# Kernel tuning notes

Measured on AMD Instinct MI355X. Metric: run time of the kernel, lower is better.

## Reference

```python
import jax, jax.numpy as jnp
import numpy as np

H = 2          # h_dim (hard-coded in PPIModel)
L = 4          # n_hid rgcn layers
R = 16         # num_rels
B = 8          # num_bases
N = 1_000_000  # num_nodes
E = 16_000_000 # num_edges


def setup_inputs() -> dict:
    key = jax.random.key(0)
    ks = jax.random.split(key, 10)
    features = jax.random.normal(ks[0], (N * H,), dtype=jnp.float32)
    edge_src = jax.random.randint(ks[1], (E,), 0, N)
    edge_dst = jax.random.randint(ks[2], (E,), 0, N)
    edge_type = jax.random.randint(ks[3], (E,), 0, R)
    norm = jax.random.uniform(ks[4], (E, 1), dtype=jnp.float32)
    # Basis-decomposition params per layer: W_r = sum_b comp[r,b] * V[b]
    V = jax.random.normal(ks[5], (L, B, H, H), dtype=jnp.float32) / np.sqrt(H)
    comp = jax.random.normal(ks[6], (L, R, B), dtype=jnp.float32) / np.sqrt(B)
    bias = jnp.zeros((L, H), dtype=jnp.float32)  # DGL RelGraphConv h_bias (default bias=True)
    w_mlp = jax.random.normal(ks[7], (1, N * H), dtype=jnp.float32) / np.sqrt(N * H)
    b_mlp = jnp.zeros((1,), dtype=jnp.float32)
    return dict(features=features, norm=norm, V=V, comp=comp, bias=bias,
                w_mlp=w_mlp, b_mlp=b_mlp,
                edge_src=edge_src, edge_dst=edge_dst, edge_type=edge_type)


def reference(features, norm, V, comp, bias, w_mlp, b_mlp, edge_src, edge_dst, edge_type):
    x = features.reshape(-1, H)          # [N, 2]
    skip = x
    for i in range(L):
        # relation weights from bases: [R, H, H]
        W = jnp.einsum('rb,bio->rio', comp[i], V[i])
        # message per edge: gather src feats, apply relation weight, scale by norm
        msg = jnp.einsum('ei,eio->eo', x[edge_src], W[edge_type]) * norm  # [E, 2]
        # scatter-sum to destination nodes
        h = jax.ops.segment_sum(msg, edge_dst, num_segments=N) + bias[i]  # [N, 2]
        if i < L - 1:
            h = jax.nn.relu(h)
        x = h
        if i % 2 == 1:
            x = x + skip
            skip = x
    flat = x.reshape(1, N * H)           # [1, 2N]
    logit = flat @ w_mlp.T + b_mlp       # [1, 1]
    return jax.nn.sigmoid(logit)
```

## Files before the change

### kernel.cpp

```cpp
#include <hip/hip_runtime.h>
#include <hip/hip_bf16.h>
#include <hip/hip_fp16.h>

#define HD 2
#define LAYERS 4
#define RELS 16
#define BASES 8

#define NB   512
#define BSH  11
#define SBLK 512
#define TPB  256


__global__ void prep_kernel(const float* __restrict__ V, const float* __restrict__ comp,
                            float* __restrict__ W, float* __restrict__ acc) {
    int idx = threadIdx.x;
    if (idx < LAYERS * RELS * 4) {
        int l  = idx >> 6;
        int r  = (idx >> 2) & (RELS - 1);
        int io = idx & 3;
        float s = 0.f;
        for (int b = 0; b < BASES; ++b)
            s += comp[(l * RELS + r) * BASES + b] * V[(l * BASES + b) * 4 + io];
        W[idx] = s;
    }
    if (idx == 0) *acc = 0.f;
}

__global__ void finalize_kernel(const float* __restrict__ acc,
                                const float* __restrict__ b_mlp,
                                float* __restrict__ out) {
    float v = *acc + b_mlp[0];
    out[0] = 1.f / (1.f + expf(-v));
}

__global__ __launch_bounds__(TPB) void f2h_kernel(const float2* __restrict__ f,
                                                  __half2* __restrict__ h, int N) {
    int i = blockIdx.x * TPB + threadIdx.x;
    int stride = gridDim.x * TPB;
    for (; i < N; i += stride)
        h[i] = __float22half2_rn(f[i]);
}


__global__ __launch_bounds__(TPB) void hist_kernel(const int* __restrict__ dst,
                                                   unsigned* __restrict__ blockhist,
                                                   int E, int per) {
    __shared__ unsigned hist[NB];
    for (int i = threadIdx.x; i < NB; i += TPB) hist[i] = 0u;
    __syncthreads();
    int blk = blockIdx.x;
    int e0 = blk * per;
    int e1 = min(e0 + per, E);
    const int4* dst4 = (const int4*)dst;
    int g0 = e0 >> 2, g1 = e1 >> 2;
    for (int g = g0 + threadIdx.x; g < g1; g += TPB) {
        int4 d = dst4[g];
        atomicAdd(&hist[((unsigned)d.x) >> BSH], 1u);
        atomicAdd(&hist[((unsigned)d.y) >> BSH], 1u);
        atomicAdd(&hist[((unsigned)d.z) >> BSH], 1u);
        atomicAdd(&hist[((unsigned)d.w) >> BSH], 1u);
    }
    for (int e = (g1 << 2) + threadIdx.x; e < e1; e += TPB)
        atomicAdd(&hist[((unsigned)dst[e]) >> BSH], 1u);
    __syncthreads();
    for (int i = threadIdx.x; i < NB; i += TPB)
        blockhist[(size_t)blk * NB + i] = hist[i];
}

__global__ __launch_bounds__(TPB) void colscan_kernel(unsigned* __restrict__ blockhist,
                                                      unsigned* __restrict__ totals) {
    int bucket = blockIdx.x;
    int t = threadIdx.x;
    unsigned v0 = blockhist[(size_t)(2 * t)     * NB + bucket];
    unsigned v1 = blockhist[(size_t)(2 * t + 1) * NB + bucket];
    unsigned run = v0 + v1;
    __shared__ unsigned s[TPB];
    s[t] = run;
    __syncthreads();
    for (int off = 1; off < TPB; off <<= 1) {
        unsigned x = (t >= off) ? s[t - off] : 0u;
        __syncthreads();
        s[t] += x;
        __syncthreads();
    }
    unsigned base = s[t] - run;
    blockhist[(size_t)(2 * t)     * NB + bucket] = base;
    blockhist[(size_t)(2 * t + 1) * NB + bucket] = base + v0;
    if (t == TPB - 1) totals[bucket] = s[TPB - 1];
}

__global__ __launch_bounds__(TPB) void scan_kernel(const unsigned* __restrict__ totals,
                                                   unsigned* __restrict__ base) {
    int t = threadIdx.x;
    unsigned v0 = totals[2 * t];
    unsigned v1 = totals[2 * t + 1];
    unsigned run = v0 + v1;
    __shared__ unsigned s[TPB];
    s[t] = run;
    __syncthreads();
    for (int off = 1; off < TPB; off <<= 1) {
        unsigned x = (t >= off) ? s[t - off] : 0u;
        __syncthreads();
        s[t] += x;
        __syncthreads();
    }
    unsigned b0 = s[t] - run;
    base[2 * t]     = b0;
    base[2 * t + 1] = b0 + v0;
    if (t == TPB - 1) base[NB] = s[TPB - 1];
}

__global__ __launch_bounds__(TPB) void scatter_kernel(const int* __restrict__ src,
                                                      const int* __restrict__ dst,
                                                      const int* __restrict__ typ,
                                                      const float* __restrict__ norm,
                                                      const unsigned* __restrict__ blockhist,
                                                      const unsigned* __restrict__ base,
                                                      uint2* __restrict__ packed,
                                                      int E, int per) {
    __shared__ unsigned cnt[NB];
    int blk = blockIdx.x;
    for (int i = threadIdx.x; i < NB; i += TPB)
        cnt[i] = blockhist[(size_t)blk * NB + i] + base[i];
    __syncthreads();
    int e0 = blk * per;
    int e1 = min(e0 + per, E);
    const int4*   src4 = (const int4*)src;
    const int4*   dst4 = (const int4*)dst;
    const int4*   typ4 = (const int4*)typ;
    const float4* nrm4 = (const float4*)norm;
    int g0 = e0 >> 2, g1 = e1 >> 2;

#define PUT(SS, DD, TT, NN)                                                       \
    {                                                                             \
        unsigned _d = (unsigned)(DD);                                             \
        unsigned _bucket = _d >> BSH;                                             \
        unsigned _pos = atomicAdd(&cnt[_bucket], 1u);                             \
        unsigned _w1 = (_d & ((1u << BSH) - 1u)) | (((unsigned)(TT)) << 12) |     \
                       ((unsigned)__half_as_ushort(__float2half_rn(NN)) << 16);   \
        packed[_pos] = make_uint2((unsigned)(SS), _w1);                           \
    }

    for (int g = g0 + threadIdx.x; g < g1; g += TPB) {
        int4 s = src4[g];
        int4 d = dst4[g];
        int4 t = typ4[g];
        float4 nm = nrm4[g];
        PUT(s.x, d.x, t.x, nm.x)
        PUT(s.y, d.y, t.y, nm.y)
        PUT(s.z, d.z, t.z, nm.z)
        PUT(s.w, d.w, t.w, nm.w)
    }
    for (int e = (g1 << 2) + threadIdx.x; e < e1; e += TPB)
        PUT(src[e], dst[e], typ[e], norm[e])
#undef PUT
}

__global__ __launch_bounds__(TPB) void bucket_edge_kernel(
    const uint2* __restrict__ packed,
    const unsigned* __restrict__ base,
    const __half2* __restrict__ xh,
    const float* __restrict__ Wl,
    const float* __restrict__ bias2,
    const __half2* __restrict__ skiph,
    __half2* __restrict__ outh,
    const float2* __restrict__ w2,
    float* __restrict__ acc,
    int N, int do_relu)
{
    __shared__ float acc0[1 << BSH];
    __shared__ float acc1[1 << BSH];
    __shared__ float sW[64];
    __shared__ float wred[4];

    int t = threadIdx.x;
#pragma unroll
    for (int k = 0; k < (1 << BSH) / TPB; ++k) {
        acc0[k * TPB + t] = 0.f;
        acc1[k * TPB + t] = 0.f;
    }
    if (t < 64) sW[t] = Wl[t];
    __syncthreads();

    int b  = blockIdx.x;
    int e0 = (int)base[b];
    int e1 = (int)base[b + 1];

    const unsigned long long* pk8 = (const unsigned long long*)packed;

    for (int e = e0 + t; e < e1; e += 2 * TPB) {
        unsigned long long q0 = __builtin_nontemporal_load(&pk8[e]);
        int e2 = e + TPB;
        bool has2 = e2 < e1;
        unsigned long long q1 = has2 ? __builtin_nontemporal_load(&pk8[e2]) : 0ull;

        unsigned s0i = (unsigned)(q0 & 0xffffffffu);
        unsigned w10 = (unsigned)(q0 >> 32);
        unsigned s1i = (unsigned)(q1 & 0xffffffffu);
        unsigned w11 = (unsigned)(q1 >> 32);

        __half2 hv0 = xh[s0i];
        __half2 hv1 = has2 ? xh[s1i] : __half2{};

        {
            float xv0 = __low2float(hv0), xv1 = __high2float(hv0);
            unsigned dof = w10 & ((1u << BSH) - 1u);
            int wb = (int)((w10 >> 12) & 15u) << 2;
            float nm = __half2float(__ushort_as_half((unsigned short)(w10 >> 16)));
            float m0 = (xv0 * sW[wb + 0] + xv1 * sW[wb + 2]) * nm;
            float m1 = (xv0 * sW[wb + 1] + xv1 * sW[wb + 3]) * nm;
            atomicAdd(&acc0[dof], m0);
            atomicAdd(&acc1[dof], m1);
        }
        if (has2) {
            float xv0 = __low2float(hv1), xv1 = __high2float(hv1);
            unsigned dof = w11 & ((1u << BSH) - 1u);
            int wb = (int)((w11 >> 12) & 15u) << 2;
            float nm = __half2float(__ushort_as_half((unsigned short)(w11 >> 16)));
            float m0 = (xv0 * sW[wb + 0] + xv1 * sW[wb + 2]) * nm;
            float m1 = (xv0 * sW[wb + 1] + xv1 * sW[wb + 3]) * nm;
            atomicAdd(&acc0[dof], m0);
            atomicAdd(&acc1[dof], m1);
        }
    }
    __syncthreads();

    float b0 = bias2[0], b1 = bias2[1];
    int nodeBase = b << BSH;
    float part = 0.f;
#pragma unroll
    for (int k = 0; k < (1 << BSH) / TPB; ++k) {
        int i = k * TPB + t;
        int node = nodeBase + i;
        if (node < N) {
            float v0 = acc0[i] + b0;
            float v1 = acc1[i] + b1;
            if (do_relu) { v0 = fmaxf(v0, 0.f); v1 = fmaxf(v1, 0.f); }
            if (skiph) {
                __half2 sv = skiph[node];
                v0 += __low2float(sv); v1 += __high2float(sv);
            }
            if (outh) outh[node] = __float22half2_rn(make_float2(v0, v1));
            if (w2)   { float2 wv = w2[node]; part += v0 * wv.x + v1 * wv.y; }
        }
    }
    if (w2) {
        for (int off = 32; off > 0; off >>= 1) part += __shfl_down(part, off, 64);
        int lane = t & 63, wv = t >> 6;
        if (lane == 0) wred[wv] = part;
        __syncthreads();
        if (t == 0) atomicAdd(acc, wred[0] + wred[1] + wred[2] + wred[3]);
    }
}


__global__ void zero_kernel(float4* __restrict__ p, int n4) {
    int i = blockIdx.x * blockDim.x + threadIdx.x;
    int stride = gridDim.x * blockDim.x;
    for (; i < n4; i += stride) p[i] = make_float4(0.f, 0.f, 0.f, 0.f);
}

__global__ __launch_bounds__(256) void edge_kernel(
    const float* __restrict__ x, const int* __restrict__ src,
    const int* __restrict__ dst, const int* __restrict__ typ,
    const float* __restrict__ norm, const float* __restrict__ Wl,
    float* __restrict__ h, int E)
{
    __shared__ float sW[64];
    if (threadIdx.x < 64) sW[threadIdx.x] = Wl[threadIdx.x];
    __syncthreads();
    const float2* __restrict__ x2 = (const float2*)x;
    int tid = blockIdx.x * blockDim.x + threadIdx.x;
    int stride = gridDim.x * blockDim.x;
    for (int e = tid; e < E; e += stride) {
        int s = src[e], d = dst[e], t = typ[e];
        float nm = norm[e];
        float2 xv = x2[s];
        int wb = t << 2;
        float m0 = (xv.x * sW[wb + 0] + xv.y * sW[wb + 2]) * nm;
        float m1 = (xv.x * sW[wb + 1] + xv.y * sW[wb + 3]) * nm;
        atomicAdd(&h[2 * (size_t)d],     m0);
        atomicAdd(&h[2 * (size_t)d + 1], m1);
    }
}

__global__ void node_kernel(const float* __restrict__ h, const float* __restrict__ bias_l,
                            const float* __restrict__ skip, float* __restrict__ xout,
                            int N, int do_relu)
{
    float b0 = bias_l[0], b1 = bias_l[1];
    const float2* __restrict__ h2 = (const float2*)h;
    const float2* __restrict__ s2 = (const float2*)skip;
    float2* __restrict__ o2 = (float2*)xout;
    int i = blockIdx.x * blockDim.x + threadIdx.x;
    int stride = gridDim.x * blockDim.x;
    for (; i < N; i += stride) {
        float2 v = h2[i];
        v.x += b0; v.y += b1;
        if (do_relu) { v.x = fmaxf(v.x, 0.f); v.y = fmaxf(v.y, 0.f); }
        if (skip) { float2 sv = s2[i]; v.x += sv.x; v.y += sv.y; }
        o2[i] = v;
    }
}

__global__ __launch_bounds__(256) void dot_kernel(const float* __restrict__ a,
                                                  const float* __restrict__ b,
                                                  float* __restrict__ acc, int n)
{
    int i = blockIdx.x * blockDim.x + threadIdx.x;
    int stride = gridDim.x * blockDim.x;
    float s = 0.f;
    int n4 = n >> 2;
    const float4* __restrict__ a4 = (const float4*)a;
    const float4* __restrict__ b4 = (const float4*)b;
    for (int g = i; g < n4; g += stride) {
        float4 av = a4[g], bv = b4[g];
        s += av.x * bv.x + av.y * bv.y + av.z * bv.z + av.w * bv.w;
    }
    for (int e = (n4 << 2) + i; e < n; e += stride) s += a[e] * b[e];
    for (int off = 32; off > 0; off >>= 1) s += __shfl_down(s, off, 64);
    __shared__ float wsum[4];
    int lane = threadIdx.x & 63, wv = threadIdx.x >> 6;
    if (lane == 0) wsum[wv] = s;
    __syncthreads();
    if (threadIdx.x == 0) atomicAdd(acc, wsum[0] + wsum[1] + wsum[2] + wsum[3]);
}


static inline size_t align256(size_t x) { return (x + 255) & ~(size_t)255; }

extern "C" void kernel_launch(void* const* d_in, const int* in_sizes, int n_in,
                              void* d_out, int out_size, void* d_ws, size_t ws_size,
                              hipStream_t stream) {
    const float* features = (const float*)d_in[0];
    const float* norm     = (const float*)d_in[1];
    const float* V        = (const float*)d_in[2];
    const float* comp     = (const float*)d_in[3];
    const float* bias     = (const float*)d_in[4];
    const float* w_mlp    = (const float*)d_in[5];
    const float* b_mlp    = (const float*)d_in[6];
    const int*   esrc     = (const int*)d_in[7];
    const int*   edst     = (const int*)d_in[8];
    const int*   etyp     = (const int*)d_in[9];

    int NH = in_sizes[0];
    int N  = NH / 2;
    int E  = in_sizes[7];

    char* ws = (char*)d_ws;
    size_t oA    = 0;
    size_t oB    = align256(oA + (size_t)NH * 4);
    size_t oC    = align256(oB + (size_t)NH * 4);
    size_t oFH   = align256(oC + (size_t)NH * 4);
    size_t oAH   = align256(oFH + (size_t)N * 4);
    size_t oBH   = align256(oAH + (size_t)N * 4);
    size_t oCH   = align256(oBH + (size_t)N * 4);
    size_t oW    = align256(oCH + (size_t)N * 4);
    size_t oAcc  = align256(oW + 1024);
    size_t oBase = align256(oAcc + 4);
    size_t oTot  = align256(oBase + (size_t)(NB + 1) * 4);
    size_t oHist = align256(oTot + (size_t)NB * 4);
    size_t oPack = align256(oHist + (size_t)SBLK * NB * 4);
    size_t REQ   = oPack + (size_t)E * 8;

    float* A    = (float*)(ws + oA);
    float* B    = (float*)(ws + oB);
    float* C    = (float*)(ws + oC);
    float* W    = (float*)(ws + oW);
    float* acc  = (float*)(ws + oAcc);

    prep_kernel<<<1, 256, 0, stream>>>(V, comp, W, acc);

    if (ws_size >= REQ && N <= (1 << 20)) {
        __half2* FH = (__half2*)(ws + oFH);
        __half2* AH = (__half2*)(ws + oAH);
        __half2* BH = (__half2*)(ws + oBH);
        __half2* CH = (__half2*)(ws + oCH);
        unsigned* base      = (unsigned*)(ws + oBase);
        unsigned* totals    = (unsigned*)(ws + oTot);
        unsigned* blockhist = (unsigned*)(ws + oHist);
        uint2*    packed    = (uint2*)(ws + oPack);

        int per = (((E + SBLK - 1) / SBLK) + 3) & ~3;

        int cb = min((N + TPB - 1) / TPB, 2048);
        f2h_kernel    <<<cb,   TPB, 0, stream>>>((const float2*)features, FH, N);
        hist_kernel   <<<SBLK, TPB, 0, stream>>>(edst, blockhist, E, per);
        colscan_kernel<<<NB,   TPB, 0, stream>>>(blockhist, totals);
        scan_kernel   <<<1,    TPB, 0, stream>>>(totals, base);
        scatter_kernel<<<SBLK, TPB, 0, stream>>>(esrc, edst, etyp, norm,
                                                 blockhist, base, packed, E, per);

        int nbkt = (N + (1 << BSH) - 1) >> BSH;
        const float2* w2 = (const float2*)w_mlp;

        bucket_edge_kernel<<<nbkt, TPB, 0, stream>>>(packed, base, FH, W + 0,
            bias + 0, nullptr, AH, nullptr, acc, N, 1);
        bucket_edge_kernel<<<nbkt, TPB, 0, stream>>>(packed, base, AH, W + 64,
            bias + 2, FH, BH, nullptr, acc, N, 1);
        bucket_edge_kernel<<<nbkt, TPB, 0, stream>>>(packed, base, BH, W + 128,
            bias + 4, nullptr, CH, nullptr, acc, N, 1);
        bucket_edge_kernel<<<nbkt, TPB, 0, stream>>>(packed, base, CH, W + 192,
            bias + 6, BH, nullptr, w2, acc, N, 0);
    } else {
        int zb = (NH / 4 + 255) / 256;
        int eb = (E / 4 + 255) / 256;
        int nb = (N + 255) / 256;
        int db = (NH / 4 + 255) / 256;

        zero_kernel<<<zb, 256, 0, stream>>>((float4*)A, NH / 4);
        edge_kernel<<<eb, 256, 0, stream>>>(features, esrc, edst, etyp, norm, W + 0, A, E);
        node_kernel<<<nb, 256, 0, stream>>>(A, bias + 0, nullptr, A, N, 1);

        zero_kernel<<<zb, 256, 0, stream>>>((float4*)B, NH / 4);
        edge_kernel<<<eb, 256, 0, stream>>>(A, esrc, edst, etyp, norm, W + 64, B, E);
        node_kernel<<<nb, 256, 0, stream>>>(B, bias + 2, features, B, N, 1);

        zero_kernel<<<zb, 256, 0, stream>>>((float4*)C, NH / 4);
        edge_kernel<<<eb, 256, 0, stream>>>(B, esrc, edst, etyp, norm, W + 128, C, E);
        node_kernel<<<nb, 256, 0, stream>>>(C, bias + 4, nullptr, C, N, 1);

        zero_kernel<<<zb, 256, 0, stream>>>((float4*)A, NH / 4);
        edge_kernel<<<eb, 256, 0, stream>>>(C, esrc, edst, etyp, norm, W + 192, A, E);
        node_kernel<<<nb, 256, 0, stream>>>(A, bias + 6, B, A, N, 0);

        dot_kernel<<<db, 256, 0, stream>>>(A, w_mlp, acc, NH);
    }

    finalize_kernel<<<1, 1, 0, stream>>>(acc, b_mlp, (float*)d_out);
}
```

Measured before the change: 1.133 ms.

## Bucket edges by destination tile and source block for gather locality

Replaces the 512 destination buckets of 2048 nodes with a two-level key: 16K-node destination tiles, each subdivided by 2048-node source blocks, giving 32768 sort keys. Edges within a tile are then ordered by source block, which should make the per-edge feature gathers more cache-local. The edge kernel now runs one 1024-thread block per tile with larger LDS accumulators. The price is much larger histograms (128KB LDS per block, bigger blockhist and colscan work) and far fewer edge-kernel blocks (about 62), which may underfill the GPU.

```diff
diff --git a/kernel.cpp b/kernel.cpp
--- a/kernel.cpp
+++ b/kernel.cpp
@@ -7,10 +7,17 @@
 #define RELS 16
 #define BASES 8
 
-#define NB   512
-#define BSH  11
-#define SBLK 512
-#define TPB  256
+#define TSH    14
+#define TILEN  (1 << TSH)
+#define SBH    11
+#define SRCB_BITS 9
+#define KEYS   32768
+#define SBLK   192
+#define TPB    256
+#define ETPB   1024
+
+static const int KEYS_LDS_BYTES = KEYS * 4;
+static const int EDGE_LDS_BYTES = 2 * TILEN * 4;
 
 
 __global__ void prep_kernel(const float* __restrict__ V, const float* __restrict__ comp,
@@ -44,72 +51,76 @@
 }
 
 
-__global__ __launch_bounds__(TPB) void hist_kernel(const int* __restrict__ dst,
+__global__ __launch_bounds__(TPB) void hist_kernel(const int* __restrict__ src,
+                                                   const int* __restrict__ dst,
                                                    unsigned* __restrict__ blockhist,
                                                    int E, int per) {
-    __shared__ unsigned hist[NB];
-    for (int i = threadIdx.x; i < NB; i += TPB) hist[i] = 0u;
+    extern __shared__ unsigned hist[];
+    for (int i = threadIdx.x; i < KEYS; i += TPB) hist[i] = 0u;
     __syncthreads();
     int blk = blockIdx.x;
     int e0 = blk * per;
     int e1 = min(e0 + per, E);
+    const int4* src4 = (const int4*)src;
     const int4* dst4 = (const int4*)dst;
     int g0 = e0 >> 2, g1 = e1 >> 2;
     for (int g = g0 + threadIdx.x; g < g1; g += TPB) {
+        int4 s = src4[g];
         int4 d = dst4[g];
-        atomicAdd(&hist[((unsigned)d.x) >> BSH], 1u);
-        atomicAdd(&hist[((unsigned)d.y) >> BSH], 1u);
-        atomicAdd(&hist[((unsigned)d.z) >> BSH], 1u);
-        atomicAdd(&hist[((unsigned)d.w) >> BSH], 1u);
+        atomicAdd(&hist[((((unsigned)d.x) >> TSH) << SRCB_BITS) | (((unsigned)s.x) >> SBH)], 1u);
+        atomicAdd(&hist[((((unsigned)d.y) >> TSH) << SRCB_BITS) | (((unsigned)s.y) >> SBH)], 1u);
+        atomicAdd(&hist[((((unsigned)d.z) >> TSH) << SRCB_BITS) | (((unsigned)s.z) >> SBH)], 1u);
+        atomicAdd(&hist[((((unsigned)d.w) >> TSH) << SRCB_BITS) | (((unsigned)s.w) >> SBH)], 1u);
     }
     for (int e = (g1 << 2) + threadIdx.x; e < e1; e += TPB)
-        atomicAdd(&hist[((unsigned)dst[e]) >> BSH], 1u);
-    __syncthreads();
-    for (int i = threadIdx.x; i < NB; i += TPB)
-        blockhist[(size_t)blk * NB + i] = hist[i];
-}
-
-__global__ __launch_bounds__(TPB) void colscan_kernel(unsigned* __restrict__ blockhist,
-                                                      unsigned* __restrict__ totals) {
-    int bucket = blockIdx.x;
+        atomicAdd(&hist[((((unsigned)dst[e]) >> TSH) << SRCB_BITS) | (((unsigned)src[e]) >> SBH)], 1u);
+    __syncthreads();
+    for (int i = threadIdx.x; i < KEYS; i += TPB)
+        blockhist[(size_t)blk * KEYS + i] = hist[i];
+}
+
+__global__ __launch_bounds__(64) void colscan_kernel(unsigned* __restrict__ blockhist,
+                                                     unsigned* __restrict__ totals) {
+    int key = blockIdx.x;
     int t = threadIdx.x;
-    unsigned v0 = blockhist[(size_t)(2 * t)     * NB + bucket];
-    unsigned v1 = blockhist[(size_t)(2 * t + 1) * NB + bucket];
-    unsigned run = v0 + v1;
-    __shared__ unsigned s[TPB];
-    s[t] = run;
-    __syncthreads();
-    for (int off = 1; off < TPB; off <<= 1) {
-        unsigned x = (t >= off) ? s[t - off] : 0u;
-        __syncthreads();
-        s[t] += x;
-        __syncthreads();
-    }
-    unsigned base = s[t] - run;
-    blockhist[(size_t)(2 * t)     * NB + bucket] = base;
-    blockhist[(size_t)(2 * t + 1) * NB + bucket] = base + v0;
-    if (t == TPB - 1) totals[bucket] = s[TPB - 1];
-}
-
-__global__ __launch_bounds__(TPB) void scan_kernel(const unsigned* __restrict__ totals,
-                                                   unsigned* __restrict__ base) {
+    unsigned v0 = blockhist[(size_t)(3 * t)     * KEYS + key];
+    unsigned v1 = blockhist[(size_t)(3 * t + 1) * KEYS + key];
+    unsigned v2 = blockhist[(size_t)(3 * t + 2) * KEYS + key];
+    unsigned run = v0 + v1 + v2;
+    unsigned v = run;
+    for (int o = 1; o < 64; o <<= 1) {
+        unsigned u = __shfl_up(v, o, 64);
+        if (t >= o) v += u;
+    }
+    unsigned excl = v - run;
+    blockhist[(size_t)(3 * t)     * KEYS + key] = excl;
+    blockhist[(size_t)(3 * t + 1) * KEYS + key] = excl + v0;
+    blockhist[(size_t)(3 * t + 2) * KEYS + key] = excl + v0 + v1;
+    if (t == 63) totals[key] = v;
+}
+
+__global__ __launch_bounds__(ETPB) void scan_kernel(const unsigned* __restrict__ totals,
+                                                    unsigned* __restrict__ base) {
+    __shared__ unsigned wpart[ETPB / 64];
     int t = threadIdx.x;
-    unsigned v0 = totals[2 * t];
-    unsigned v1 = totals[2 * t + 1];
-    unsigned run = v0 + v1;
-    __shared__ unsigned s[TPB];
-    s[t] = run;
-    __syncthreads();
-    for (int off = 1; off < TPB; off <<= 1) {
-        unsigned x = (t >= off) ? s[t - off] : 0u;
-        __syncthreads();
-        s[t] += x;
-        __syncthreads();
-    }
-    unsigned b0 = s[t] - run;
-    base[2 * t]     = b0;
-    base[2 * t + 1] = b0 + v0;
-    if (t == TPB - 1) base[NB] = s[TPB - 1];
+    unsigned run = 0;
+    for (int k = 0; k < 32; ++k) run += totals[t * 32 + k];
+    unsigned lane = t & 63, wv = t >> 6;
+    unsigned v = run;
+    for (int o = 1; o < 64; o <<= 1) {
+        unsigned u = __shfl_up(v, o, 64);
+        if (lane >= (unsigned)o) v += u;
+    }
+    if (lane == 63) wpart[wv] = v;
+    __syncthreads();
+    unsigned wbase = 0;
+    for (int w = 0; w < (int)(ETPB / 64); ++w) if ((unsigned)w < wv) wbase += wpart[w];
+    unsigned e = wbase + v - run;
+    for (int k = 0; k < 32; ++k) {
+        base[t * 32 + k] = e;
+        e += totals[t * 32 + k];
+    }
+    if (t == ETPB - 1) base[KEYS] = e;
 }
 
 __global__ __launch_bounds__(TPB) void scatter_kernel(const int* __restrict__ src,
@@ -120,10 +131,10 @@
                                                       const unsigned* __restrict__ base,
                                                       uint2* __restrict__ packed,
                                                       int E, int per) {
-    __shared__ unsigned cnt[NB];
+    extern __shared__ unsigned cnt[];
     int blk = blockIdx.x;
-    for (int i = threadIdx.x; i < NB; i += TPB)
-        cnt[i] = blockhist[(size_t)blk * NB + i] + base[i];
+    for (int i = threadIdx.x; i < KEYS; i += TPB)
+        cnt[i] = blockhist[(size_t)blk * KEYS + i] + base[i];
     __syncthreads();
     int e0 = blk * per;
     int e1 = min(e0 + per, E);
@@ -133,14 +144,17 @@
     const float4* nrm4 = (const float4*)norm;
     int g0 = e0 >> 2, g1 = e1 >> 2;
 
-#define PUT(SS, DD, TT, NN)                                                       \
-    {                                                                             \
-        unsigned _d = (unsigned)(DD);                                             \
-        unsigned _bucket = _d >> BSH;                                             \
-        unsigned _pos = atomicAdd(&cnt[_bucket], 1u);                             \
-        unsigned _w1 = (_d & ((1u << BSH) - 1u)) | (((unsigned)(TT)) << 12) |     \
-                       ((unsigned)__half_as_ushort(__float2half_rn(NN)) << 16);   \
-        packed[_pos] = make_uint2((unsigned)(SS), _w1);                           \
+#define PUT(SS, DD, TT, NN)                                                        \
+    {                                                                              \
+        unsigned _s = (unsigned)(SS);                                              \
+        unsigned _d = (unsigned)(DD);                                              \
+        unsigned _key = ((_d >> TSH) << SRCB_BITS) | (_s >> SBH);                  \
+        unsigned _pos = atomicAdd(&cnt[_key], 1u);                                 \
+        unsigned _doff = _d & (TILEN - 1u);                                        \
+        unsigned _w0 = _s | (((unsigned)(TT)) << 20) | ((_doff & 0xFFu) << 24);    \
+        unsigned _w1 = (_doff >> 8) |                                              \
+                       ((unsigned)__half_as_ushort(__float2half_rn(NN)) << 16);    \
+        packed[_pos] = make_uint2(_w0, _w1);                                       \
     }
 
     for (int g = g0 + threadIdx.x; g < g1; g += TPB) {
@@ -158,8 +172,8 @@
 #undef PUT
 }
 
-__global__ __launch_bounds__(TPB) void bucket_edge_kernel(
-    const uint2* __restrict__ packed,
+__global__ __launch_bounds__(ETPB) void edge_tile_kernel(
+    const unsigned long long* __restrict__ rec8,
     const unsigned* __restrict__ base,
     const __half2* __restrict__ xh,
     const float* __restrict__ Wl,
@@ -170,69 +184,43 @@
     float* __restrict__ acc,
     int N, int do_relu)
 {
-    __shared__ float acc0[1 << BSH];
-    __shared__ float acc1[1 << BSH];
+    extern __shared__ float dsm[];
+    float* acc0 = dsm;
+    float* acc1 = dsm + TILEN;
     __shared__ float sW[64];
-    __shared__ float wred[4];
+    __shared__ float wred[ETPB / 64];
 
     int t = threadIdx.x;
-#pragma unroll
-    for (int k = 0; k < (1 << BSH) / TPB; ++k) {
-        acc0[k * TPB + t] = 0.f;
-        acc1[k * TPB + t] = 0.f;
-    }
+    for (int i = t; i < TILEN; i += ETPB) { acc0[i] = 0.f; acc1[i] = 0.f; }
     if (t < 64) sW[t] = Wl[t];
     __syncthreads();
 
-    int b  = blockIdx.x;
-    int e0 = (int)base[b];
-    int e1 = (int)base[b + 1];
-
-    const unsigned long long* pk8 = (const unsigned long long*)packed;
-
-    for (int e = e0 + t; e < e1; e += 2 * TPB) {
-        unsigned long long q0 = __builtin_nontemporal_load(&pk8[e]);
-        int e2 = e + TPB;
-        bool has2 = e2 < e1;
-        unsigned long long q1 = has2 ? __builtin_nontemporal_load(&pk8[e2]) : 0ull;
-
-        unsigned s0i = (unsigned)(q0 & 0xffffffffu);
-        unsigned w10 = (unsigned)(q0 >> 32);
-        unsigned s1i = (unsigned)(q1 & 0xffffffffu);
-        unsigned w11 = (unsigned)(q1 >> 32);
-
-        __half2 hv0 = xh[s0i];
-        __half2 hv1 = has2 ? xh[s1i] : __half2{};
-
-        {
-            float xv0 = __low2float(hv0), xv1 = __high2float(hv0);
-            unsigned dof = w10 & ((1u << BSH) - 1u);
-            int wb = (int)((w10 >> 12) & 15u) << 2;
-            float nm = __half2float(__ushort_as_half((unsigned short)(w10 >> 16)));
-            float m0 = (xv0 * sW[wb + 0] + xv1 * sW[wb + 2]) * nm;
-            float m1 = (xv0 * sW[wb + 1] + xv1 * sW[wb + 3]) * nm;
-            atomicAdd(&acc0[dof], m0);
-            atomicAdd(&acc1[dof], m1);
-        }
-        if (has2) {
-            float xv0 = __low2float(hv1), xv1 = __high2float(hv1);
-            unsigned dof = w11 & ((1u << BSH) - 1u);
-            int wb = (int)((w11 >> 12) & 15u) << 2;
-            float nm = __half2float(__ushort_as_half((unsigned short)(w11 >> 16)));
-            float m0 = (xv0 * sW[wb + 0] + xv1 * sW[wb + 2]) * nm;
-            float m1 = (xv0 * sW[wb + 1] + xv1 * sW[wb + 3]) * nm;
-            atomicAdd(&acc0[dof], m0);
-            atomicAdd(&acc1[dof], m1);
-        }
+    int tile = blockIdx.x;
+    unsigned e0 = base[tile << SRCB_BITS];
+    unsigned e1 = base[min((tile + 1) << SRCB_BITS, KEYS)];
+
+    for (unsigned e = e0 + t; e < e1; e += ETPB) {
+        unsigned long long q = __builtin_nontemporal_load(&rec8[e]);
+        unsigned w0 = (unsigned)q;
+        unsigned w1 = (unsigned)(q >> 32);
+        unsigned src  = w0 & 0xFFFFFu;
+        int      wb   = (int)((w0 >> 20) & 15u) << 2;
+        unsigned doff = (w0 >> 24) | ((w1 & 0x3Fu) << 8);
+        float    nm   = __half2float(__ushort_as_half((unsigned short)(w1 >> 16)));
+        __half2  hv   = xh[src];
+        float x0 = __low2float(hv), x1 = __high2float(hv);
+        float m0 = (x0 * sW[wb + 0] + x1 * sW[wb + 2]) * nm;
+        float m1 = (x0 * sW[wb + 1] + x1 * sW[wb + 3]) * nm;
+        atomicAdd(&acc0[doff], m0);
+        atomicAdd(&acc1[doff], m1);
     }
     __syncthreads();
 
     float b0 = bias2[0], b1 = bias2[1];
-    int nodeBase = b << BSH;
+    int nodeBase = tile << TSH;
     float part = 0.f;
-#pragma unroll
-    for (int k = 0; k < (1 << BSH) / TPB; ++k) {
-        int i = k * TPB + t;
+    for (int k = 0; k < TILEN / ETPB; ++k) {
+        int i = k * ETPB + t;
         int node = nodeBase + i;
         if (node < N) {
             float v0 = acc0[i] + b0;
@@ -247,11 +235,14 @@
         }
     }
     if (w2) {
-        for (int off = 32; off > 0; off >>= 1) part += __shfl_down(part, off, 64);
-        int lane = t & 63, wv = t >> 6;
-        if (lane == 0) wred[wv] = part;
+        for (int o = 32; o > 0; o >>= 1) part += __shfl_down(part, o, 64);
+        if ((t & 63) == 0) wred[t >> 6] = part;
         __syncthreads();
-        if (t == 0) atomicAdd(acc, wred[0] + wred[1] + wred[2] + wred[3]);
+        if (t == 0) {
+            float s = 0.f;
+            for (int w = 0; w < (int)(ETPB / 64); ++w) s += wred[w];
+            atomicAdd(acc, s);
+        }
     }
 }
 
@@ -350,26 +341,24 @@
     int E  = in_sizes[7];
 
     char* ws = (char*)d_ws;
-    size_t oA    = 0;
-    size_t oB    = align256(oA + (size_t)NH * 4);
-    size_t oC    = align256(oB + (size_t)NH * 4);
-    size_t oFH   = align256(oC + (size_t)NH * 4);
+    size_t oW    = 0;
+    size_t oAcc  = align256(oW + 1024);
+    size_t oBase = align256(oAcc + 4);
+    size_t oTot  = align256(oBase + (size_t)(KEYS + 1) * 4);
+    size_t oFH   = align256(oTot + (size_t)KEYS * 4);
     size_t oAH   = align256(oFH + (size_t)N * 4);
     size_t oBH   = align256(oAH + (size_t)N * 4);
     size_t oCH   = align256(oBH + (size_t)N * 4);
-    size_t oW    = align256(oCH + (size_t)N * 4);
-    size_t oAcc  = align256(oW + 1024);
-    size_t oBase = align256(oAcc + 4);
-    size_t oTot  = align256(oBase + (size_t)(NB + 1) * 4);
-    size_t oHist = align256(oTot + (size_t)NB * 4);
-    size_t oPack = align256(oHist + (size_t)SBLK * NB * 4);
+    size_t oHist = align256(oCH + (size_t)N * 4);
+    size_t oPack = align256(oHist + (size_t)SBLK * KEYS * 4);
     size_t REQ   = oPack + (size_t)E * 8;
 
-    float* A    = (float*)(ws + oA);
-    float* B    = (float*)(ws + oB);
-    float* C    = (float*)(ws + oC);
-    float* W    = (float*)(ws + oW);
-    float* acc  = (float*)(ws + oAcc);
+    float* A = (float*)(ws + oFH);
+    float* B = (float*)(ws + oBH);
+    float* C = (float*)(ws + oPack);
+
+    float* W   = (float*)(ws + oW);
+    float* acc = (float*)(ws + oAcc);
 
     prep_kernel<<<1, 256, 0, stream>>>(V, comp, W, acc);
 
@@ -382,27 +371,42 @@
         unsigned* totals    = (unsigned*)(ws + oTot);
         unsigned* blockhist = (unsigned*)(ws + oHist);
         uint2*    packed    = (uint2*)(ws + oPack);
+        unsigned long long* packed8 = (unsigned long long*)packed;
 
         int per = (((E + SBLK - 1) / SBLK) + 3) & ~3;
+        int ntiles = (N + TILEN - 1) / TILEN;
+
+        static bool attr_done = false;
+        if (!attr_done) {
+            (void)hipFuncSetAttribute((const void*)hist_kernel,
+                                      hipFuncAttributeMaxDynamicSharedMemorySize,
+                                      KEYS_LDS_BYTES);
+            (void)hipFuncSetAttribute((const void*)scatter_kernel,
+                                      hipFuncAttributeMaxDynamicSharedMemorySize,
+                                      KEYS_LDS_BYTES);
+            (void)hipFuncSetAttribute((const void*)edge_tile_kernel,
+                                      hipFuncAttributeMaxDynamicSharedMemorySize,
+                                      EDGE_LDS_BYTES);
+            attr_done = true;
+        }
 
         int cb = min((N + TPB - 1) / TPB, 2048);
         f2h_kernel    <<<cb,   TPB, 0, stream>>>((const float2*)features, FH, N);
-        hist_kernel   <<<SBLK, TPB, 0, stream>>>(edst, blockhist, E, per);
-        colscan_kernel<<<NB,   TPB, 0, stream>>>(blockhist, totals);
-        scan_kernel   <<<1,    TPB, 0, stream>>>(totals, base);
-        scatter_kernel<<<SBLK, TPB, 0, stream>>>(esrc, edst, etyp, norm,
-                                                 blockhist, base, packed, E, per);
-
-        int nbkt = (N + (1 << BSH) - 1) >> BSH;
+        hist_kernel   <<<SBLK, TPB, KEYS_LDS_BYTES, stream>>>(esrc, edst, blockhist, E, per);
+        colscan_kernel<<<KEYS, 64,  0, stream>>>(blockhist, totals);
+        scan_kernel   <<<1,    ETPB, 0, stream>>>(totals, base);
+        scatter_kernel<<<SBLK, TPB, KEYS_LDS_BYTES, stream>>>(
+            esrc, edst, etyp, norm, blockhist, base, packed, E, per);
+
         const float2* w2 = (const float2*)w_mlp;
 
-        bucket_edge_kernel<<<nbkt, TPB, 0, stream>>>(packed, base, FH, W + 0,
+        edge_tile_kernel<<<ntiles, ETPB, EDGE_LDS_BYTES, stream>>>(packed8, base, FH, W + 0,
             bias + 0, nullptr, AH, nullptr, acc, N, 1);
-        bucket_edge_kernel<<<nbkt, TPB, 0, stream>>>(packed, base, AH, W + 64,
+        edge_tile_kernel<<<ntiles, ETPB, EDGE_LDS_BYTES, stream>>>(packed8, base, AH, W + 64,
             bias + 2, FH, BH, nullptr, acc, N, 1);
-        bucket_edge_kernel<<<nbkt, TPB, 0, stream>>>(packed, base, BH, W + 128,
+        edge_tile_kernel<<<ntiles, ETPB, EDGE_LDS_BYTES, stream>>>(packed8, base, BH, W + 128,
             bias + 4, nullptr, CH, nullptr, acc, N, 1);
-        bucket_edge_kernel<<<nbkt, TPB, 0, stream>>>(packed, base, CH, W + 192,
+        edge_tile_kernel<<<ntiles, ETPB, EDGE_LDS_BYTES, stream>>>(packed8, base, CH, W + 192,
             bias + 6, BH, nullptr, w2, acc, N, 0);
     } else {
         int zb = (NH / 4 + 255) / 256;
```

Result: slower. 3.656 ms (+222.8%).
